# Optimization experiments

Measured on AMD Instinct MI355X. Metric: run time of the kernel, lower is better.

## Reference

```python
import jax, jax.numpy as jnp
import numpy as np
from jax import lax

NEG = -1e30  # safe -inf surrogate (avoids nan grads)
CTC_WEIGHT = 0.3


def _excl_cumsum(e):
    # exclusive cumsum along last axis: (..., U) -> (..., U+1)
    c = jnp.cumsum(e, axis=-1)
    return jnp.concatenate([jnp.zeros_like(c[..., :1]), c], axis=-1)


def _rnnt_loss(log_probs, targets, frame_len, tgt_len, blank):
    """RNNT forward DP. log_probs: (B,T,U+1,V) log-softmaxed. Returns per-seq NLL (B,)."""
    B, T, U1, V = log_probs.shape
    blank_lp = log_probs[..., blank]  # (B,T,U1)
    emit = jnp.take_along_axis(log_probs[:, :, :U1 - 1, :],
                               targets[:, None, :, None], axis=3)[..., 0]  # (B,T,U)
    # alpha[0,u] = sum_{j<u} emit[0,j]
    alpha0 = _excl_cumsum(emit[:, 0])  # (B,U1)

    def step(alpha_prev, inp):
        blank_prev, emit_t = inp  # (B,U1), (B,U)
        a = alpha_prev + blank_prev
        # alpha[t,u] = LSE(a_u, alpha[t,u-1] + emit[t,u-1]) solved in closed form:
        # alpha[t,u] = E[u] + cumLSE_{k<=u}(a_k - E[k]),  E = exclusive cumsum of emit
        E = _excl_cumsum(emit_t)
        alpha_t = E + lax.associative_scan(jnp.logaddexp, a - E, axis=-1)
        return alpha_t, alpha_t

    xs = (jnp.swapaxes(blank_lp[:, :-1], 0, 1), jnp.swapaxes(emit[:, 1:], 0, 1))
    _, alphas = lax.scan(step, alpha0, xs)
    alphas = jnp.concatenate([alpha0[None], alphas], axis=0)  # (T,B,U1)
    bi = jnp.arange(B)
    t_idx = frame_len - 1
    ll = alphas[t_idx, bi, tgt_len] + blank_lp[bi, t_idx, tgt_len]
    return -ll


def _ctc_loss(log_probs, targets, frame_len, tgt_len, blank):
    """CTC forward DP. log_probs: (B,T,V) log-softmaxed. Returns per-seq NLL (B,)."""
    B, T, V = log_probs.shape
    U = targets.shape[1]
    S = 2 * U + 1
    ext = jnp.full((B, S), blank, dtype=targets.dtype).at[:, 1::2].set(targets)  # (B,S)
    lp_ext = jnp.take_along_axis(log_probs, ext[:, None, :], axis=2)  # (B,T,S)
    ext_m2 = jnp.pad(ext[:, :-2], ((0, 0), (2, 0)), constant_values=blank)
    can_skip = (jnp.arange(S)[None, :] >= 2) & (ext != blank) & (ext != ext_m2)
    alpha0 = jnp.full((B, S), NEG).at[:, 0].set(lp_ext[:, 0, 0]).at[:, 1].set(lp_ext[:, 0, 1])

    def step(alpha, lp_t):
        p1 = jnp.pad(alpha[:, :-1], ((0, 0), (1, 0)), constant_values=NEG)
        p2 = jnp.where(can_skip,
                       jnp.pad(alpha[:, :-2], ((0, 0), (2, 0)), constant_values=NEG), NEG)
        m = jnp.maximum(jnp.maximum(alpha, p1), p2)
        new = lp_t + m + jnp.log(jnp.exp(alpha - m) + jnp.exp(p1 - m) + jnp.exp(p2 - m))
        return new, new

    _, alphas = lax.scan(step, alpha0, jnp.swapaxes(lp_ext, 0, 1)[1:])
    alphas = jnp.concatenate([alpha0[None], alphas], axis=0)  # (T,B,S)
    bi = jnp.arange(B)
    t_idx = frame_len - 1
    a_last = alphas[t_idx, bi, 2 * tgt_len]
    a_prev = alphas[t_idx, bi, 2 * tgt_len - 1]
    return -jnp.logaddexp(a_last, a_prev)


def setup_inputs() -> dict:
    key = jax.random.key(0)
    ks = jax.random.split(key, 9)
    B, T, U, V = 4, 200, 50, 1024
    D, H = 512, 640
    return {
        "x_enc": jax.random.normal(ks[0], (B, T, D), jnp.float32),
        "x_dec": jax.random.normal(ks[1], (B, U + 1, H), jnp.float32),
        "target": jax.random.randint(ks[2], (B, U), 0, V - 1),  # excludes blank = V-1
        "frame_length": jax.random.randint(ks[3], (B,), 150, T + 1).astype(jnp.int32),
        "target_length": jax.random.randint(ks[4], (B,), 30, U + 1).astype(jnp.int32),
        "W_ctc": jax.random.normal(ks[5], (D, V), jnp.float32) * 0.02,
        "b_ctc": jnp.zeros((V,), jnp.float32),
        "W_enc": jax.random.normal(ks[6], (D, H), jnp.float32) * 0.02,
        "W_pred": jax.random.normal(ks[7], (H, H), jnp.float32) * 0.02,
        "b_joint": jnp.zeros((H,), jnp.float32),
        "W_out": jax.random.normal(ks[8], (H, V), jnp.float32) * 0.02,
        "b_out": jnp.zeros((V,), jnp.float32),
    }


def reference(x_enc, x_dec, target, frame_length, target_length,
              W_ctc, b_ctc, W_enc, W_pred, b_joint, W_out, b_out):
    B = x_enc.shape[0]
    V = W_ctc.shape[1]
    blank = V - 1
    # CTC head: linear + log_softmax over vocab
    ctc_lp = jax.nn.log_softmax(x_enc @ W_ctc + b_ctc, axis=-1)  # (B,T,V)
    # Joiner: enc proj (B,T,1,J) + pred proj (B,1,U+1,J) -> tanh -> vocab
    joint = jnp.tanh(jnp.einsum('btd,dj->btj', x_enc, W_enc)[:, :, None, :]
                     + jnp.einsum('buh,hj->buj', x_dec, W_pred)[:, None, :, :]
                     + b_joint)  # (B,T,U+1,J)
    rnnt_lp = jax.nn.log_softmax(jnp.einsum('btuj,jv->btuv', joint, W_out) + b_out, axis=-1)
    rnnt = _rnnt_loss(rnnt_lp, target, frame_length, target_length, blank).mean()
    ctc = _ctc_loss(ctc_lp, target, frame_length, target_length, blank).sum() / B
    return rnnt + CTC_WEIGHT * ctc
```

## Files before the change

kernel.cpp:

```cpp
#include <hip/hip_runtime.h>
#include <hip/hip_bf16.h>

typedef __bf16 bf16_t;
typedef __attribute__((ext_vector_type(8))) __bf16 bf16x8;
typedef __attribute__((ext_vector_type(4))) float f32x4;
typedef __attribute__((ext_vector_type(8))) int i32x8;
typedef __attribute__((ext_vector_type(4))) int i32x4;

#define NEGV (-1e30f)

#define BB 4
#define TT 200
#define UU 50
#define U1 51
#define VV 1024
#define DD 512
#define HH 640
#define RTOT (BB*TT*U1)
#define NBLK 638
#define SS 101

__device__ __forceinline__ float lae(float a, float b) {
    float mx = fmaxf(a, b);
    return mx + __logf(__expf(a - mx) + __expf(b - mx));
}
__device__ __forceinline__ float lae3(float a, float b, float c) {
    float mx = fmaxf(fmaxf(a, b), c);
    return mx + __logf(__expf(a - mx) + __expf(b - mx) + __expf(c - mx));
}
__device__ __forceinline__ float tanh_rcp(float x) {
    x = fminf(fmaxf(x, -10.f), 10.f);
    float ex = __expf(2.f * x);
    float r = __builtin_amdgcn_rcpf(ex + 1.f);
    return (ex - 1.f) * r;
}

__device__ __forceinline__ void pack_out8_mx(const float* __restrict__ W, unsigned* __restrict__ Wf8,
                                             int e32)
{
    int w4   = e32 & 7;
    int l    = (e32 >> 3) & 63;
    int ksnt = e32 >> 9;
    int ks   = ksnt % 5;
    int nt   = ksnt / 5;
    int v = nt * 16 + (l & 15);
    int kb = ks * 128 + ((l >> 4) << 5) + w4 * 4;
    float f[4];
#pragma unroll
    for (int t = 0; t < 4; ++t) f[t] = W[(size_t)(kb + t) * VV + v] * 16.f;
    unsigned r = __builtin_amdgcn_cvt_pk_fp8_f32(f[0], f[1], 0, false);
    r = __builtin_amdgcn_cvt_pk_fp8_f32(f[2], f[3], r, true);
    Wf8[e32] = r;
}

__global__ void pack_all(const float* __restrict__ Wenc, const float* __restrict__ Wpred,
                         const float* __restrict__ Wctc, const float* __restrict__ Wout,
                         bf16_t* __restrict__ FEnc, bf16_t* __restrict__ FPred,
                         bf16_t* __restrict__ FCtc, unsigned* __restrict__ FOut8,
                         float* __restrict__ out)
{
    if (blockIdx.x == 0 && threadIdx.x == 0) out[0] = 0.f;
    if (blockIdx.x >= 616) {
        int e32 = (blockIdx.x - 616) * 256 + threadIdx.x;
        pack_out8_mx(Wout, FOut8, e32);
        return;
    }
    int f = blockIdx.x * 256 + threadIdx.x;
    const float* W; bf16_t* Wf; int K32, N;
    if (f < 40960)      { W = Wenc;  Wf = FEnc;  K32 = 16; N = 640; }
    else if (f < 92160) { f -= 40960; W = Wpred; Wf = FPred; K32 = 20; N = 640; }
    else                { f -= 92160; W = Wctc;  Wf = FCtc;  K32 = 16; N = 1024; }
    int l  = f & 63;
    int kk = (f >> 6) % K32;
    int nt = f / (64 * K32);
    int v  = nt * 16 + (l & 15);
    int kb = kk * 32 + ((l >> 4) << 2);
    bf16x8 o;
#pragma unroll
    for (int j = 0; j < 8; ++j) {
        int k = kb + (j & 3) + ((j >> 2) << 4);
        o[j] = (bf16_t)W[(size_t)k * N + v];
    }
    *(bf16x8*)&Wf[(size_t)f * 8] = o;
}

template<int K32, int L, bool LSE, int J>
__device__ void gemm_dev(const float* __restrict__ A, int M, int rowbase, int K,
                         const bf16_t* __restrict__ Wf, const float* __restrict__ bias,
                         float* __restrict__ C, float* __restrict__ lse_out, int N,
                         bf16_t* Atile, float (*ps)[8])
{
    const int tid = threadIdx.x;
#pragma unroll
    for (int it = 0; it < J * K32 / 8; ++it) {
        int fi = it * 512 + tid;
        int l = fi & 63, jk = fi >> 6;
        int j = jk / K32, kk = jk - j * K32;
        int row = rowbase + j * 16 + (l & 15);
        if (row > M - 1) row = M - 1;
        int c0 = kk * 32 + ((l >> 4) << 2);
        const float4 a0 = *(const float4*)&A[(size_t)row * K + c0];
        const float4 a1 = *(const float4*)&A[(size_t)row * K + c0 + 16];
        bf16x8 v;
        v[0] = (bf16_t)a0.x; v[1] = (bf16_t)a0.y; v[2] = (bf16_t)a0.z; v[3] = (bf16_t)a0.w;
        v[4] = (bf16_t)a1.x; v[5] = (bf16_t)a1.y; v[6] = (bf16_t)a1.z; v[7] = (bf16_t)a1.w;
        *(bf16x8*)&Atile[(size_t)fi * 8] = v;
    }
    __syncthreads();

    const int l = tid & 63, w = tid >> 6;
    const int lrow = l & 15, lhi = l >> 4;

    f32x4 acc[J][L];
#pragma unroll
    for (int j = 0; j < J; ++j)
#pragma unroll
        for (int li = 0; li < L; ++li) acc[j][li] = f32x4{0.f, 0.f, 0.f, 0.f};

    for (int kk = 0; kk < K32; ++kk) {
        bf16x8 a[J];
#pragma unroll
        for (int j = 0; j < J; ++j)
            a[j] = *(const bf16x8*)&Atile[(size_t)(((j * K32 + kk) * 64 + l) * 8)];
#pragma unroll
        for (int li = 0; li < L; ++li) {
            bf16x8 b = *(const bf16x8*)&Wf[(size_t)(((w * L + li) * K32 + kk) * 64 + l) * 8];
#pragma unroll
            for (int j = 0; j < J; ++j)
                acc[j][li] = __builtin_amdgcn_mfma_f32_16x16x32_bf16(a[j], b, acc[j][li], 0, 0, 0);
        }
    }

    float se[J][4];
    if (LSE) {
#pragma unroll
        for (int j = 0; j < J; ++j)
#pragma unroll
            for (int i = 0; i < 4; ++i) se[j][i] = 0.f;
    }
#pragma unroll
    for (int j = 0; j < J; ++j)
#pragma unroll
        for (int li = 0; li < L; ++li) {
            int col = (w * L + li) * 16 + lrow;
            float bv = bias ? bias[col] : 0.f;
#pragma unroll
            for (int i = 0; i < 4; ++i) {
                int grow = rowbase + 16 * j + lhi * 4 + i;
                float x = acc[j][li][i] + bv;
                if (grow < M) C[(size_t)grow * N + col] = x;
                if (LSE) se[j][i] += __expf(x);
            }
        }
    if (LSE) {
#pragma unroll
        for (int d = 1; d < 16; d <<= 1)
#pragma unroll
            for (int j = 0; j < J; ++j)
#pragma unroll
                for (int i = 0; i < 4; ++i) se[j][i] += __shfl_xor(se[j][i], d);
        if (lrow == 0) {
#pragma unroll
            for (int j = 0; j < J; ++j)
#pragma unroll
                for (int i = 0; i < 4; ++i) ps[16 * j + lhi * 4 + i][w] = se[j][i];
        }
        __syncthreads();
        if (tid < J * 16) {
            float s = 0.f;
#pragma unroll
            for (int w0 = 0; w0 < 8; ++w0) s += ps[tid][w0];
            int grow = rowbase + tid;
            if (grow < M) lse_out[grow] = __logf(s);
        }
    }
}

__global__ __launch_bounds__(512)
void mfma_gemm3(const float* __restrict__ x_enc, const float* __restrict__ x_dec,
                const bf16_t* __restrict__ FEnc, const bf16_t* __restrict__ FPred,
                const bf16_t* __restrict__ FCtc, const float* __restrict__ b_ctc,
                float* __restrict__ enc_proj, float* __restrict__ pred_proj,
                float* __restrict__ ctc_logits, float* __restrict__ ctc_lse)
{
    __shared__ bf16_t Atile[2560 * 8];
    __shared__ float ps[64][8];
    int blk = blockIdx.x;
    if (blk < 50)
        gemm_dev<16, 5, false, 1>(x_enc, 800, blk * 16, 512, FEnc, nullptr, enc_proj, nullptr, 640, Atile, ps);
    else if (blk < 57)
        gemm_dev<20, 5, false, 2>(x_dec, 204, (blk - 50) * 32, 640, FPred, nullptr, pred_proj, nullptr, 640, Atile, ps);
    else
        gemm_dev<16, 8, true, 1>(x_enc, 800, (blk - 57) * 16, 512, FCtc, b_ctc, ctc_logits, ctc_lse, 1024, Atile, ps);
}

__global__ __launch_bounds__(512)
void joint_gemm(const float* __restrict__ enc,
                const float* __restrict__ pred,
                const float* __restrict__ bj,
                const unsigned* __restrict__ Wf8,
                const float* __restrict__ bo,
                const int* __restrict__ target,
                float* __restrict__ blank_buf, float* __restrict__ emit_buf,
                const float* __restrict__ ctc_logits, const float* __restrict__ ctc_lse,
                const int* __restrict__ frame_len, const int* __restrict__ tgt_len,
                float* __restrict__ out)
{
    __shared__ __align__(16) char smem[82944];
    __shared__ const float* ep[64];
    __shared__ const float* pp[64];
    const int tid = threadIdx.x;
    const int blk = blockIdx.x;

    if (blk < 4) {
        const int b = blk;
        float* lpE = (float*)smem;
        float* lpO = (float*)smem + 208;
        for (int i = tid; i < TT; i += 512) {
            int bt = b * TT + i;
            lpE[i] = ctc_logits[(size_t)bt * VV + (VV - 1)] - ctc_lse[bt];
        }
        for (int i = tid; i < TT * UU; i += 512) {
            int t = i / UU, uu = i - t * UU;
            int bt = b * TT + t;
            lpO[uu * 209 + t] = ctc_logits[(size_t)bt * VV + target[b * UU + uu]] - ctc_lse[bt];
        }
        __syncthreads();
        if (tid >= 64) return;
        const int u = tid;
        const int fl = frame_len[b], tl = tgt_len[b];
        const bool acte = (u <= 50);
        const bool acto = (u < 50);
        bool skip = (u >= 1 && u < UU) ? (target[b * UU + u] != target[b * UU + u - 1]) : false;
        const float* orow = lpO + u * 209;
        float old_e = (u == 0) ? lpE[0] : NEGV;
        float old_o = (u == 0) ? orow[0] : NEGV;
        float Esave = (fl == 1) ? old_e : NEGV;
        float Osave = (fl == 1) ? old_o : NEGV;

        for (int t0 = 1; t0 <= 193; t0 += 8) {
            float bo8[8], be8[8];
#pragma unroll
            for (int s = 0; s < 8; ++s) { bo8[s] = orow[t0 + s]; be8[s] = lpE[t0 + s]; }
#pragma unroll
            for (int s = 0; s < 8; ++s) {
                int t = t0 + s;
                float prev_o = __shfl_up(old_o, 1);
                if (u == 0) prev_o = NEGV;
                float ne = be8[s] + lae(old_e, prev_o);
                float no = bo8[s] + lae3(old_o, old_e, skip ? prev_o : NEGV);
                old_e = acte ? ne : NEGV;
                old_o = acto ? no : NEGV;
                bool hv = (t == fl - 1) && (t < TT);
                Esave = hv ? old_e : Esave;
                Osave = hv ? old_o : Osave;
            }
        }
        float a_last = __shfl(Esave, tl);
        float a_prev = __shfl(Osave, tl - 1);
        if (u == 0) atomicAdd(out, -0.075f * lae(a_last, a_prev));
        return;
    }

    const int jb = blk - 4;
    char* tile = smem;
    char* Afrag8 = smem + 41984;
    const int l = tid & 63, w = tid >> 6;
    const int lrow = l & 15, lhi = l >> 4;

    if (tid < 64) {
        int r = jb * 64 + tid; if (r > RTOT - 1) r = RTOT - 1;
        int b = r / (TT * U1); int rem = r - b * (TT * U1);
        int t = rem / U1;      int u = rem - t * U1;
        ep[tid] = enc + (size_t)(b * TT + t) * HH;
        pp[tid] = pred + (size_t)(b * U1 + u) * HH;
    }
    __syncthreads();

#pragma unroll 4
    for (int it = 0; it < 20; ++it) {
        int i = it * 512 + tid;
        int row = i / 160;
        int c4 = i - row * 160;
        int c0 = c4 * 4;
        const float4 e4 = *(const float4*)&ep[row][c0];
        const float4 p4 = *(const float4*)&pp[row][c0];
        const float4 q4 = *(const float4*)&bj[c0];
        float f0 = tanh_rcp(e4.x + p4.x + q4.x);
        float f1 = tanh_rcp(e4.y + p4.y + q4.y);
        float f2 = tanh_rcp(e4.z + p4.z + q4.z);
        float f3 = tanh_rcp(e4.w + p4.w + q4.w);
        unsigned r0 = __builtin_amdgcn_cvt_pk_fp8_f32(f0, f1, 0, false);
        unsigned v = __builtin_amdgcn_cvt_pk_fp8_f32(f2, f3, r0, true);
        *(unsigned*)&tile[row * 656 + c0] = v;
    }
    __syncthreads();

#pragma unroll
    for (int it = 0; it < 5; ++it) {
        int c = it * 512 + tid;
        int lA = c & 63;
        int plane = c >> 6;
        int h = plane & 1;
        int jks = plane >> 1;
        int ks = jks % 5;
        int j = jks / 5;
        int row = j * 16 + (lA & 15);
        int kbase = ks * 128 + ((lA >> 4) << 5) + h * 16;
        uint4 v = *(const uint4*)&tile[row * 656 + kbase];
        *(uint4*)&Afrag8[(size_t)c * 16] = v;
    }
    __syncthreads();

    f32x4 acc[4][8];
#pragma unroll
    for (int j = 0; j < 4; ++j)
#pragma unroll
        for (int li = 0; li < 8; ++li) acc[j][li] = f32x4{0.f, 0.f, 0.f, 0.f};

    const char* Bp8 = (const char*)Wf8 + (size_t)(w * 8) * 10240 + (size_t)l * 32;

    const int rot = jb % 5;
    auto kstep = [&](int ks) {
        i32x8 a[4];
#pragma unroll
        for (int j = 0; j < 4; ++j) {
            i32x4 lo = *(const i32x4*)(Afrag8 + (size_t)(((j * 5 + ks) * 2 + 0) * 1024 + l * 16));
            i32x4 hi = *(const i32x4*)(Afrag8 + (size_t)(((j * 5 + ks) * 2 + 1) * 1024 + l * 16));
            a[j][0] = lo[0]; a[j][1] = lo[1]; a[j][2] = lo[2]; a[j][3] = lo[3];
            a[j][4] = hi[0]; a[j][5] = hi[1]; a[j][6] = hi[2]; a[j][7] = hi[3];
        }
#pragma unroll
        for (int li = 0; li < 8; ++li) {
            i32x8 b = *(const i32x8*)(Bp8 + (size_t)li * 10240 + (size_t)ks * 2048);
#pragma unroll
            for (int j = 0; j < 4; ++j)
                acc[j][li] = __builtin_amdgcn_mfma_scale_f32_16x16x128_f8f6f4(
                    a[j], b, acc[j][li], 0, 0,
                    0, 0x7F7F7F7F, 0, 0x7F7F7F7F);
        }
    };
    for (int ks0 = rot; ks0 < 5; ++ks0) kstep(ks0);
    for (int ks0 = 0; ks0 < rot; ++ks0) kstep(ks0);

    int tg[4][4];
#pragma unroll
    for (int j = 0; j < 4; ++j)
#pragma unroll
        for (int i = 0; i < 4; ++i) {
            int r = jb * 64 + 16 * j + lhi * 4 + i; if (r > RTOT - 1) r = RTOT - 1;
            int b = r / (TT * U1); int rem = r - b * (TT * U1);
            int u = rem % U1;
            tg[j][i] = (u < UU) ? target[b * UU + u] : -1;
        }

    float se[4][4], ee[4][4], bbv[4][4];
#pragma unroll
    for (int j = 0; j < 4; ++j)
#pragma unroll
        for (int i = 0; i < 4; ++i) { se[j][i] = 0.f; ee[j][i] = NEGV; bbv[j][i] = NEGV; }

#pragma unroll
    for (int li = 0; li < 8; ++li) {
        int col = (w * 8 + li) * 16 + lrow;
        float bv = bo[col];
#pragma unroll
        for (int j = 0; j < 4; ++j)
#pragma unroll
            for (int i = 0; i < 4; ++i) {
                float x = acc[j][li][i] * 0.0625f + bv;
                se[j][i] += __expf(x);
                if (col == tg[j][i]) ee[j][i] = x;
            }
    }
    if (w == 7) {
        float bv = bo[1023];
#pragma unroll
        for (int j = 0; j < 4; ++j)
#pragma unroll
            for (int i = 0; i < 4; ++i) {
                float x = acc[j][7][i] * 0.0625f + bv;
                if (lrow == 15) bbv[j][i] = x;
            }
    }
#pragma unroll
    for (int d = 1; d < 16; d <<= 1)
#pragma unroll
        for (int j = 0; j < 4; ++j)
#pragma unroll
            for (int i = 0; i < 4; ++i) {
                se[j][i] += __shfl_xor(se[j][i], d);
                ee[j][i] = fmaxf(ee[j][i], __shfl_xor(ee[j][i], d));
                bbv[j][i] = fmaxf(bbv[j][i], __shfl_xor(bbv[j][i], d));
            }

    __syncthreads();
    float (*ps)[8] = (float (*)[8])(Afrag8);
    float (*pe)[8] = (float (*)[8])(Afrag8 + 2048);
    float (*pb)[8] = (float (*)[8])(Afrag8 + 4096);
    if (lrow == 0) {
#pragma unroll
        for (int j = 0; j < 4; ++j)
#pragma unroll
            for (int i = 0; i < 4; ++i) {
                int r = 16 * j + lhi * 4 + i;
                ps[r][w] = se[j][i]; pe[r][w] = ee[j][i]; pb[r][w] = bbv[j][i];
            }
    }
    __syncthreads();
    if (tid < 64) {
        float s = 0.f, e = NEGV, bq = NEGV;
#pragma unroll
        for (int w0 = 0; w0 < 8; ++w0) {
            s += ps[tid][w0];
            e = fmaxf(e, pe[tid][w0]);
            bq = fmaxf(bq, pb[tid][w0]);
        }
        float lse = __logf(s);
        int gid = jb * 64 + tid;
        if (gid < RTOT) {
            blank_buf[gid] = bq - lse;
            emit_buf[gid]  = e - lse;
        }
    }
}

__global__ __launch_bounds__(512)
void dp_rnnt(const float* __restrict__ blank_buf, const float* __restrict__ emit_buf,
             const int* __restrict__ frame_len, const int* __restrict__ tgt_len,
             float* __restrict__ out)
{
    __shared__ __align__(16) float sm[28416];
    const int b = blockIdx.x;
    const int tid = threadIdx.x;

    float2* pk = (float2*)sm;
    for (int i = tid; i < TT * U1; i += 512) {
        int t = i / U1, uu = i - t * U1;
        float bl = blank_buf[(b * TT + t) * U1 + uu];
        float em = emit_buf[(b * TT + t) * U1 + uu];
        pk[uu * 217 + t + 8] = make_float2(bl, em);
    }
    __syncthreads();
    if (tid >= 64) return;
    const int u = tid;
    const int fl = frame_len[b], tl = tgt_len[b];
    const int dh = fl - 1 + tl;
    const bool isTL = (u == tl);
    const bool act = (u < U1);
    float A = (u == 0) ? 0.f : NEGV;
    float Asave = (dh == 0 && isTL) ? A : NEGV;
    const float2* prow = pk + u * 217;

    for (int d0 = 1; d0 <= 249; d0 += 8) {
        int tb = d0 - 1 - u;
        int tc = tb; if (tc < -8) tc = -8; if (tc > 200) tc = 200;
        float2 buf[8];
#pragma unroll
        for (int s = 0; s < 8; ++s) buf[s] = prow[tc + 8 + s];
#pragma unroll
        for (int s = 0; s < 8; ++s) {
            int d = d0 + s;
            int t_new = d - u;
            float2 be = buf[s];
            float vshare = A + be.y;
            float left = __shfl_up(vshare, 1);
            if (u == 0) left = NEGV;
            float up = (t_new >= 1) ? (A + be.x) : NEGV;
            float Anew = lae(up, left);
            bool valid = act && (t_new >= 0) && (t_new < TT);
            A = valid ? Anew : A;
            Asave = (isTL && d == dh) ? A : Asave;
        }
    }
    if (isTL && act) {
        float bl = prow[(fl - 1) + 8].x;
        atomicAdd(out, -0.25f * (Asave + bl));
    }
}

extern "C" void kernel_launch(void* const* d_in, const int* in_sizes, int n_in,
                              void* d_out, int out_size, void* d_ws, size_t ws_size,
                              hipStream_t stream)
{
    const float* x_enc   = (const float*)d_in[0];
    const float* x_dec   = (const float*)d_in[1];
    const int*   target  = (const int*)d_in[2];
    const int*   frame_l = (const int*)d_in[3];
    const int*   tgt_l   = (const int*)d_in[4];
    const float* W_ctc   = (const float*)d_in[5];
    const float* b_ctc   = (const float*)d_in[6];
    const float* W_enc   = (const float*)d_in[7];
    const float* W_pred  = (const float*)d_in[8];
    const float* b_joint = (const float*)d_in[9];
    const float* W_out   = (const float*)d_in[10];
    const float* b_out   = (const float*)d_in[11];
    float* out = (float*)d_out;

    float* wsf        = (float*)d_ws;
    float* enc_proj   = wsf;
    float* pred_proj  = wsf + 512000;
    float* ctc_logits = wsf + 642560;
    float* ctc_lse    = wsf + 1461760;
    float* blank_buf  = wsf + 1462592;
    float* emit_buf   = wsf + 1503424;
    unsigned* FOut8 = (unsigned*)(wsf + 1544272);
    bf16_t* FEnc  = (bf16_t*)(wsf + 1708112);
    bf16_t* FPred = (bf16_t*)(wsf + 1871952);
    bf16_t* FCtc  = (bf16_t*)(wsf + 2076752);

    pack_all<<<1256, 256, 0, stream>>>(W_enc, W_pred, W_ctc, W_out,
                                       FEnc, FPred, FCtc, FOut8, out);
    mfma_gemm3<<<107, 512, 0, stream>>>(x_enc, x_dec, FEnc, FPred, FCtc, b_ctc,
                                        enc_proj, pred_proj, ctc_logits, ctc_lse);
    joint_gemm<<<NBLK + 4, 512, 0, stream>>>(enc_proj, pred_proj, b_joint, FOut8, b_out,
                                             target, blank_buf, emit_buf,
                                             ctc_logits, ctc_lse, frame_l, tgt_l, out);
    dp_rnnt<<<4, 512, 0, stream>>>(blank_buf, emit_buf, frame_l, tgt_l, out);
}
```

Measured before the change: 144.0 us.

## Split CTC GEMM across column halves with atomic exp-sum, trim RNNT DP loop

The CTC logits GEMM is split into two column halves per row tile, doubling its block count from 50 to 100. Each half accumulates its partial exp-sum into a zeroed buffer with atomicAdd, and the log is taken later in the CTC DP blocks. Separately, the RNNT diagonal DP loop now stops at the per-sequence last needed diagonal instead of a fixed bound. This trades extra atomics and a reload of the A tile per half for more parallelism in the GEMM launch. The exp-sum is not max-stabilised, so it relies on the logits staying small, as the earlier code also did.

Result: no change. 142.6 us (-0.9%).

```diff
diff --git a/kernel.cpp b/kernel.cpp
--- a/kernel.cpp
+++ b/kernel.cpp
@@ -57,9 +57,11 @@
                          const float* __restrict__ Wctc, const float* __restrict__ Wout,
                          bf16_t* __restrict__ FEnc, bf16_t* __restrict__ FPred,
                          bf16_t* __restrict__ FCtc, unsigned* __restrict__ FOut8,
-                         float* __restrict__ out)
-{
-    if (blockIdx.x == 0 && threadIdx.x == 0) out[0] = 0.f;
+                         float* __restrict__ ctc_sum, float* __restrict__ out)
+{
+    int z = blockIdx.x * 256 + threadIdx.x;
+    if (z == 0) out[0] = 0.f;
+    if (z < 832) ctc_sum[z] = 0.f;
     if (blockIdx.x >= 616) {
         int e32 = (blockIdx.x - 616) * 256 + threadIdx.x;
         pack_out8_mx(Wout, FOut8, e32);
@@ -84,11 +86,11 @@
     *(bf16x8*)&Wf[(size_t)f * 8] = o;
 }
 
-template<int K32, int L, bool LSE, int J>
+template<int K32, int L, bool SUM, int J>
 __device__ void gemm_dev(const float* __restrict__ A, int M, int rowbase, int K,
                          const bf16_t* __restrict__ Wf, const float* __restrict__ bias,
-                         float* __restrict__ C, float* __restrict__ lse_out, int N,
-                         bf16_t* Atile, float (*ps)[8])
+                         float* __restrict__ C, float* __restrict__ sum_out, int N,
+                         int colbase, bf16_t* Atile, float (*ps)[8])
 {
     const int tid = threadIdx.x;
 #pragma unroll
@@ -132,7 +134,7 @@
     }
 
     float se[J][4];
-    if (LSE) {
+    if (SUM) {
 #pragma unroll
         for (int j = 0; j < J; ++j)
 #pragma unroll
@@ -142,17 +144,17 @@
     for (int j = 0; j < J; ++j)
 #pragma unroll
         for (int li = 0; li < L; ++li) {
-            int col = (w * L + li) * 16 + lrow;
+            int col = colbase + (w * L + li) * 16 + lrow;
             float bv = bias ? bias[col] : 0.f;
 #pragma unroll
             for (int i = 0; i < 4; ++i) {
                 int grow = rowbase + 16 * j + lhi * 4 + i;
                 float x = acc[j][li][i] + bv;
                 if (grow < M) C[(size_t)grow * N + col] = x;
-                if (LSE) se[j][i] += __expf(x);
+                if (SUM) se[j][i] += __expf(x);
             }
         }
-    if (LSE) {
+    if (SUM) {
 #pragma unroll
         for (int d = 1; d < 16; d <<= 1)
 #pragma unroll
@@ -171,7 +173,7 @@
 #pragma unroll
             for (int w0 = 0; w0 < 8; ++w0) s += ps[tid][w0];
             int grow = rowbase + tid;
-            if (grow < M) lse_out[grow] = __logf(s);
+            if (grow < M) atomicAdd(&sum_out[grow], s);
         }
     }
 }
@@ -181,17 +183,22 @@
                 const bf16_t* __restrict__ FEnc, const bf16_t* __restrict__ FPred,
                 const bf16_t* __restrict__ FCtc, const float* __restrict__ b_ctc,
                 float* __restrict__ enc_proj, float* __restrict__ pred_proj,
-                float* __restrict__ ctc_logits, float* __restrict__ ctc_lse)
+                float* __restrict__ ctc_logits, float* __restrict__ ctc_sum)
 {
     __shared__ bf16_t Atile[2560 * 8];
     __shared__ float ps[64][8];
     int blk = blockIdx.x;
     if (blk < 50)
-        gemm_dev<16, 5, false, 1>(x_enc, 800, blk * 16, 512, FEnc, nullptr, enc_proj, nullptr, 640, Atile, ps);
+        gemm_dev<16, 5, false, 1>(x_enc, 800, blk * 16, 512, FEnc, nullptr, enc_proj, nullptr, 640, 0, Atile, ps);
     else if (blk < 57)
-        gemm_dev<20, 5, false, 2>(x_dec, 204, (blk - 50) * 32, 640, FPred, nullptr, pred_proj, nullptr, 640, Atile, ps);
-    else
-        gemm_dev<16, 8, true, 1>(x_enc, 800, (blk - 57) * 16, 512, FCtc, b_ctc, ctc_logits, ctc_lse, 1024, Atile, ps);
+        gemm_dev<20, 5, false, 2>(x_dec, 204, (blk - 50) * 32, 640, FPred, nullptr, pred_proj, nullptr, 640, 0, Atile, ps);
+    else {
+        int c = blk - 57;
+        int h = c / 50;
+        int rb = (c % 50) * 16;
+        gemm_dev<16, 4, true, 1>(x_enc, 800, rb, 512, FCtc + (size_t)h * 32 * 8192, b_ctc,
+                                 ctc_logits, ctc_sum, 1024, h * 512, Atile, ps);
+    }
 }
 
 __global__ __launch_bounds__(512)
@@ -202,7 +209,7 @@
                 const float* __restrict__ bo,
                 const int* __restrict__ target,
                 float* __restrict__ blank_buf, float* __restrict__ emit_buf,
-                const float* __restrict__ ctc_logits, const float* __restrict__ ctc_lse,
+                const float* __restrict__ ctc_logits, const float* __restrict__ ctc_sum,
                 const int* __restrict__ frame_len, const int* __restrict__ tgt_len,
                 float* __restrict__ out)
 {
@@ -216,14 +223,18 @@
         const int b = blk;
         float* lpE = (float*)smem;
         float* lpO = (float*)smem + 208;
+        float* lsb = (float*)smem + 208 + 50 * 209;
+        for (int i = tid; i < TT; i += 512)
+            lsb[i] = __logf(ctc_sum[b * TT + i]);
+        __syncthreads();
         for (int i = tid; i < TT; i += 512) {
             int bt = b * TT + i;
-            lpE[i] = ctc_logits[(size_t)bt * VV + (VV - 1)] - ctc_lse[bt];
+            lpE[i] = ctc_logits[(size_t)bt * VV + (VV - 1)] - lsb[i];
         }
         for (int i = tid; i < TT * UU; i += 512) {
             int t = i / UU, uu = i - t * UU;
             int bt = b * TT + t;
-            lpO[uu * 209 + t] = ctc_logits[(size_t)bt * VV + target[b * UU + uu]] - ctc_lse[bt];
+            lpO[uu * 209 + t] = ctc_logits[(size_t)bt * VV + target[b * UU + uu]] - lsb[t];
         }
         __syncthreads();
         if (tid >= 64) return;
@@ -452,7 +463,7 @@
     float Asave = (dh == 0 && isTL) ? A : NEGV;
     const float2* prow = pk + u * 217;
 
-    for (int d0 = 1; d0 <= 249; d0 += 8) {
+    for (int d0 = 1; d0 <= dh; d0 += 8) {
         int tb = d0 - 1 - u;
         int tc = tb; if (tc < -8) tc = -8; if (tc > 200) tc = 200;
         float2 buf[8];
@@ -501,7 +512,7 @@
     float* enc_proj   = wsf;
     float* pred_proj  = wsf + 512000;
     float* ctc_logits = wsf + 642560;
-    float* ctc_lse    = wsf + 1461760;
+    float* ctc_sum    = wsf + 1461760;
     float* blank_buf  = wsf + 1462592;
     float* emit_buf   = wsf + 1503424;
     unsigned* FOut8 = (unsigned*)(wsf + 1544272);
@@ -510,11 +521,11 @@
     bf16_t* FCtc  = (bf16_t*)(wsf + 2076752);
 
     pack_all<<<1256, 256, 0, stream>>>(W_enc, W_pred, W_ctc, W_out,
-                                       FEnc, FPred, FCtc, FOut8, out);
-    mfma_gemm3<<<107, 512, 0, stream>>>(x_enc, x_dec, FEnc, FPred, FCtc, b_ctc,
-                                        enc_proj, pred_proj, ctc_logits, ctc_lse);
+                                       FEnc, FPred, FCtc, FOut8, ctc_sum, out);
+    mfma_gemm3<<<157, 512, 0, stream>>>(x_enc, x_dec, FEnc, FPred, FCtc, b_ctc,
+                                        enc_proj, pred_proj, ctc_logits, ctc_sum);
     joint_gemm<<<NBLK + 4, 512, 0, stream>>>(enc_proj, pred_proj, b_joint, FOut8, b_out,
                                              target, blank_buf, emit_buf,
-                                             ctc_logits, ctc_lse, frame_l, tgt_l, out);
+                                             ctc_logits, ctc_sum, frame_l, tgt_l, out);
     dp_rnnt<<<4, 512, 0, stream>>>(blank_buf, emit_buf, frame_l, tgt_l, out);
 }
```
